# Optimization experiments

Hardware: AMD Instinct MI355X
Metric: run time of the kernel (lower is better)

## Reference

```python
import jax, jax.numpy as jnp
import numpy as np

IN_DIM = 1024
OUT_DIM = 1024


def setup_inputs() -> dict:
    key = jax.random.key(0)
    k1, k2, k3, k4 = jax.random.split(key, 4)
    B, T = 4, 2048
    x = jax.random.normal(k1, (B, T, IN_DIM), dtype=jnp.float32)
    # torch Linear stores weight as [out, in]; y = x @ W.T
    s = 1.0 / np.sqrt(IN_DIM)
    Wq = jax.random.uniform(k2, (OUT_DIM, IN_DIM), jnp.float32, -s, s)
    Wk = jax.random.uniform(k3, (OUT_DIM, IN_DIM), jnp.float32, -s, s)
    Wv = jax.random.uniform(k4, (OUT_DIM, IN_DIM), jnp.float32, -s, s)
    return {"x": x, "Wq": Wq, "Wk": Wk, "Wv": Wv}


def reference(x, Wq, Wk, Wv):
    # x: [B, T, D_in]
    q = jnp.einsum('btd,od->bto', x, Wq)   # [B, T, D_out]
    k = jnp.einsum('btd,od->bto', x, Wk)
    v = jnp.einsum('btd,od->bto', x, Wv)
    T = x.shape[1]
    scores = jnp.einsum('bqo,bko->bqk', q, k)  # [B, T, T]
    causal = jnp.tril(jnp.ones((T, T), dtype=bool))  # True = keep
    scores = jnp.where(causal, scores, -jnp.inf)
    scale = 1.0 / jnp.sqrt(jnp.asarray(k.shape[-1], scores.dtype))
    weights = jax.nn.softmax(scores * scale, axis=-1)
    # dropout_value = 0.0 -> identity
    return jnp.einsum('bqk,bko->bqo', weights, v)
```

## Files before the change

kernel.cpp:

```cpp
#include <hip/hip_runtime.h>
#include <cstdint>
#include <cstddef>

typedef __attribute__((ext_vector_type(8))) short bf16x8;
typedef __attribute__((ext_vector_type(4))) float f32x4;

#define CSCALE 0.045084220027780106f

__device__ __forceinline__ void gload_lds16(const void* g, void* l) {
  __builtin_amdgcn_global_load_lds(
      (const __attribute__((address_space(1))) unsigned int*)g,
      (__attribute__((address_space(3))) unsigned int*)l, 16, 0, 0);
}

__device__ __forceinline__ unsigned short f2bf(float f) {
  unsigned int u = __float_as_uint(f);
  return (unsigned short)((u + 0x7FFFu + ((u >> 16) & 1u)) >> 16);
}

__device__ __forceinline__ float bf2f(unsigned short u) {
  return __uint_as_float((unsigned int)u << 16);
}

__global__ void cvt_kernel(const float* __restrict__ in,
                           unsigned short* __restrict__ out, int n8) {
  int i = blockIdx.x * blockDim.x + threadIdx.x;
  if (i >= n8) return;
  const float4* p = (const float4*)in + (size_t)i * 2;
  float4 a = p[0], b = p[1];
  float vals[8] = {a.x, a.y, a.z, a.w, b.x, b.y, b.z, b.w};
  union { unsigned short u[8]; uint4 v; } r;
#pragma unroll
  for (int j = 0; j < 8; ++j) r.u[j] = f2bf(vals[j]);
  ((uint4*)out)[i] = r.v;
}

template <int MODE>
__global__ __launch_bounds__(256) void gemm_k(
    const unsigned short* __restrict__ A, const unsigned short* __restrict__ B,
    void* __restrict__ Cv) {
  constexpr int LDA = (MODE <= 1) ? 1024 : 2048;
  constexpr int LDB = (MODE <= 1) ? 1024 : (MODE == 2 ? 2048 : 8192);
  constexpr int LDC =
      (MODE == 0) ? 2048 : (MODE == 1 ? 8192 : (MODE == 2 ? 2048 : 1024));

  int arow, brow, ksteps = 32, kb = 0;
  size_t cbase;
  if constexpr (MODE == 0 || MODE == 1) {
    arow = blockIdx.x * 128;
    brow = blockIdx.y * 128;
    cbase = (size_t)arow * LDC + blockIdx.y * 128;
  } else if constexpr (MODE == 2) {
    int i = blockIdx.x, j = blockIdx.y, b = blockIdx.z;
    if (j > i) return;
    arow = b * 2048 + i * 128;
    brow = b * 2048 + j * 128;
    cbase = (size_t)(b * 2048 + i * 128) * LDC + j * 128;
  } else {
    int bm = blockIdx.x;
    int b = bm >> 4, qt = 15 - (bm & 15);
    arow = b * 2048 + qt * 128;
    brow = blockIdx.y * 128;
    kb = b * 2048;
    ksteps = (qt + 1) * 4;
    cbase = (size_t)(b * 2048 + qt * 128) * LDC + blockIdx.y * 128;
  }

  __shared__ unsigned short As[2][4096];
  __shared__ unsigned short Bs[2][4096];
  const int tid = threadIdx.x, w = tid >> 6, lane = tid & 63;
  const int l15 = lane & 15, g = lane >> 4;
  const int wm = w >> 1, wn = w & 1;
  f32x4 acc[4][4] = {};

  auto stage = [&](int buf, int k0) {
#pragma unroll
    for (int oi = 0; oi < 2; ++oi) {
      int o = w + oi * 4;
      int chunk = o * 64 + lane;
      int row = chunk >> 2, c8 = chunk & 3;
      gload_lds16(A + (size_t)(arow + row) * LDA + k0 + c8 * 8,
                  &As[buf][o * 512]);
      gload_lds16(B + (size_t)(brow + row) * LDB + kb + k0 + c8 * 8,
                  &Bs[buf][o * 512]);
    }
  };

  stage(0, 0);
  asm volatile("s_waitcnt vmcnt(0)" ::: "memory");
  __builtin_amdgcn_s_barrier();

  for (int t = 0; t < ksteps; ++t) {
    int buf = t & 1;
    if (t + 1 < ksteps) stage(buf ^ 1, (t + 1) * 32);
    bf16x8 af[4], bfr[4];
#pragma unroll
    for (int mt = 0; mt < 4; ++mt)
      af[mt] = *(const bf16x8*)&As[buf][(wm * 64 + mt * 16 + l15) * 32 + g * 8];
#pragma unroll
    for (int nt = 0; nt < 4; ++nt)
      bfr[nt] = *(const bf16x8*)&Bs[buf][(wn * 64 + nt * 16 + l15) * 32 + g * 8];
#pragma unroll
    for (int mt = 0; mt < 4; ++mt)
#pragma unroll
      for (int nt = 0; nt < 4; ++nt)
        acc[mt][nt] = __builtin_amdgcn_mfma_f32_16x16x32_bf16(
            af[mt], bfr[nt], acc[mt][nt], 0, 0, 0);
    asm volatile("s_waitcnt vmcnt(0)" ::: "memory");
    __builtin_amdgcn_s_barrier();
  }

#pragma unroll
  for (int mt = 0; mt < 4; ++mt) {
#pragma unroll
    for (int r = 0; r < 4; ++r) {
      int ro = wm * 64 + mt * 16 + g * 4 + r;
      int co = wn * 64 + l15;
      if constexpr (MODE == 3) {
        float* Cp = (float*)Cv + cbase + (size_t)ro * LDC + co;
#pragma unroll
        for (int nt = 0; nt < 4; ++nt) Cp[nt * 16] = acc[mt][nt][r];
      } else {
        unsigned short* Cp = (unsigned short*)Cv + cbase + (size_t)ro * LDC + co;
#pragma unroll
        for (int nt = 0; nt < 4; ++nt) Cp[nt * 16] = f2bf(acc[mt][nt][r]);
      }
    }
  }
}

__global__ __launch_bounds__(256) void softmax_kernel(
    unsigned short* __restrict__ S) {
  const int r = blockIdx.x * 4 + (threadIdx.x >> 6);
  const int lane = threadIdx.x & 63;
  const int q = r & 2047;
  unsigned short* row = S + (size_t)r * 2048;
  const int klen = q + 1;
  const int kmax = ((q >> 7) + 1) << 7;

  float v[4][8];
  float m = -__builtin_inff();
#pragma unroll
  for (int it = 0; it < 4; ++it) {
    int base = (lane + it * 64) * 8;
    if (base < klen) {
      bf16x8 u = *(const bf16x8*)(row + base);
#pragma unroll
      for (int e = 0; e < 8; ++e) {
        float f = bf2f((unsigned short)u[e]) * CSCALE;
        v[it][e] = (base + e <= q) ? f : -__builtin_inff();
        m = fmaxf(m, v[it][e]);
      }
    } else {
#pragma unroll
      for (int e = 0; e < 8; ++e) v[it][e] = -__builtin_inff();
    }
  }
#pragma unroll
  for (int s = 1; s < 64; s <<= 1) m = fmaxf(m, __shfl_xor(m, s));

  float lsum = 0.f;
#pragma unroll
  for (int it = 0; it < 4; ++it)
#pragma unroll
    for (int e = 0; e < 8; ++e) {
      float p = exp2f(v[it][e] - m);
      v[it][e] = p;
      lsum += p;
    }
#pragma unroll
  for (int s = 1; s < 64; s <<= 1) lsum += __shfl_xor(lsum, s);
  float inv = 1.0f / lsum;

#pragma unroll
  for (int it = 0; it < 4; ++it) {
    int base = (lane + it * 64) * 8;
    if (base < kmax) {
      union { unsigned short u[8]; uint4 x; } o;
#pragma unroll
      for (int e = 0; e < 8; ++e) o.u[e] = f2bf(v[it][e] * inv);
      *(uint4*)(row + base) = o.x;
    }
  }
}

extern "C" void kernel_launch(void* const* d_in, const int* in_sizes, int n_in,
                              void* d_out, int out_size, void* d_ws,
                              size_t ws_size, hipStream_t stream) {
  const float* x = (const float*)d_in[0];
  const float* Wq = (const float*)d_in[1];
  const float* Wk = (const float*)d_in[2];
  const float* Wv = (const float*)d_in[3];
  unsigned short* ws = (unsigned short*)d_ws;
  unsigned short* xb = ws;
  unsigned short* Wqk = ws + (size_t)(8u << 20);
  unsigned short* Wvb = ws + (size_t)(10u << 20);
  unsigned short* QKb = ws + (size_t)(11u << 20);
  unsigned short* Vtb = ws + (size_t)(27u << 20);
  unsigned short* Sb = ws + (size_t)(35u << 20);

  cvt_kernel<<<4096, 256, 0, stream>>>(x, xb, 1048576);
  cvt_kernel<<<512, 256, 0, stream>>>(Wq, Wqk, 131072);
  cvt_kernel<<<512, 256, 0, stream>>>(Wk, Wqk + (size_t)(1u << 20), 131072);
  cvt_kernel<<<512, 256, 0, stream>>>(Wv, Wvb, 131072);
  gemm_k<0><<<dim3(64, 16), 256, 0, stream>>>(xb, Wqk, QKb);
  gemm_k<1><<<dim3(8, 64), 256, 0, stream>>>(Wvb, xb, Vtb);
  gemm_k<2><<<dim3(16, 16, 4), 256, 0, stream>>>(QKb, QKb + 1024, Sb);
  softmax_kernel<<<2048, 256, 0, stream>>>(Sb);
  gemm_k<3><<<dim3(64, 8), 256, 0, stream>>>(Sb, Vtb, (float*)d_out);
}
```

Baseline: 286.7 us.

## Use 256x128 GEMM tiles with triple-buffered swizzled LDS and 8 waves

Replaces the 128x128, 4-wave, double-buffered GEMM with a 256x128 tile, 8 waves (512 threads), BK=64 and a 3-stage LDS pipeline. The LDS layout is XOR-swizzled to avoid bank conflicts, and global loads are interleaved with the MFMA phases under setprio and barriers. The three weight conversions are merged into one launch. Softmax now zero-fills up to a 256-column boundary to match the new causal tile granularity. The larger tiles cut global traffic per FLOP and hide load latency, at the cost of more wasted work on the causal diagonal and fewer blocks.

After: 259.4 us. 1.11x faster.

```diff
diff --git a/kernel.cpp b/kernel.cpp
--- a/kernel.cpp
+++ b/kernel.cpp
@@ -35,99 +35,187 @@
   ((uint4*)out)[i] = r.v;
 }
 
+__global__ void cvt3_kernel(const float* __restrict__ a,
+                            const float* __restrict__ b,
+                            const float* __restrict__ c,
+                            unsigned short* __restrict__ oa,
+                            unsigned short* __restrict__ ob,
+                            unsigned short* __restrict__ oc) {
+  int bid = blockIdx.x;
+  const float* src;
+  unsigned short* dst;
+  int base;
+  if (bid < 512) { src = a; dst = oa; base = bid; }
+  else if (bid < 1024) { src = b; dst = ob; base = bid - 512; }
+  else { src = c; dst = oc; base = bid - 1024; }
+  int i = base * 256 + threadIdx.x;
+  const float4* p = (const float4*)src + (size_t)i * 2;
+  float4 x = p[0], y = p[1];
+  float vals[8] = {x.x, x.y, x.z, x.w, y.x, y.y, y.z, y.w};
+  union { unsigned short u[8]; uint4 v; } r;
+#pragma unroll
+  for (int j = 0; j < 8; ++j) r.u[j] = f2bf(vals[j]);
+  ((uint4*)dst)[i] = r.v;
+}
+
 template <int MODE>
-__global__ __launch_bounds__(256) void gemm_k(
-    const unsigned short* __restrict__ A, const unsigned short* __restrict__ B,
-    void* __restrict__ Cv) {
+__device__ __forceinline__ void gemm8_body(const unsigned short* __restrict__ A,
+                                           const unsigned short* __restrict__ B,
+                                           void* __restrict__ Cv) {
   constexpr int LDA = (MODE <= 1) ? 1024 : 2048;
   constexpr int LDB = (MODE <= 1) ? 1024 : (MODE == 2 ? 2048 : 8192);
   constexpr int LDC =
       (MODE == 0) ? 2048 : (MODE == 1 ? 8192 : (MODE == 2 ? 2048 : 1024));
 
-  int arow, brow, ksteps = 32, kb = 0;
+  int arow, brow, nt = 16, kb = 0;
   size_t cbase;
   if constexpr (MODE == 0 || MODE == 1) {
-    arow = blockIdx.x * 128;
+    arow = blockIdx.x * 256;
     brow = blockIdx.y * 128;
     cbase = (size_t)arow * LDC + blockIdx.y * 128;
   } else if constexpr (MODE == 2) {
-    int i = blockIdx.x, j = blockIdx.y, b = blockIdx.z;
-    if (j > i) return;
-    arow = b * 2048 + i * 128;
-    brow = b * 2048 + j * 128;
-    cbase = (size_t)(b * 2048 + i * 128) * LDC + j * 128;
+    int qt = blockIdx.x, jt = blockIdx.y, b = blockIdx.z;
+    if (jt > 2 * qt + 1) return;
+    arow = b * 2048 + qt * 256;
+    brow = b * 2048 + jt * 128;
+    cbase = (size_t)arow * LDC + jt * 128;
   } else {
     int bm = blockIdx.x;
-    int b = bm >> 4, qt = 15 - (bm & 15);
-    arow = b * 2048 + qt * 128;
+    int b = bm >> 3, qt = 7 - (bm & 7);
+    arow = b * 2048 + qt * 256;
     brow = blockIdx.y * 128;
     kb = b * 2048;
-    ksteps = (qt + 1) * 4;
-    cbase = (size_t)(b * 2048 + qt * 128) * LDC + blockIdx.y * 128;
-  }
-
-  __shared__ unsigned short As[2][4096];
-  __shared__ unsigned short Bs[2][4096];
-  const int tid = threadIdx.x, w = tid >> 6, lane = tid & 63;
+    nt = (qt + 1) * 4;
+    cbase = (size_t)arow * LDC + blockIdx.y * 128;
+  }
+
+  __shared__ unsigned short As[3][256 * 64];
+  __shared__ unsigned short Bs[3][128 * 64];
+
+  const int tid = threadIdx.x;
+  const int lane = tid & 63;
   const int l15 = lane & 15, g = lane >> 4;
-  const int wm = w >> 1, wn = w & 1;
-  f32x4 acc[4][4] = {};
-
-  auto stage = [&](int buf, int k0) {
-#pragma unroll
-    for (int oi = 0; oi < 2; ++oi) {
-      int o = w + oi * 4;
-      int chunk = o * 64 + lane;
-      int row = chunk >> 2, c8 = chunk & 3;
-      gload_lds16(A + (size_t)(arow + row) * LDA + k0 + c8 * 8,
-                  &As[buf][o * 512]);
-      gload_lds16(B + (size_t)(brow + row) * LDB + kb + k0 + c8 * 8,
-                  &Bs[buf][o * 512]);
+  const int w = tid >> 6;
+  const int wm = w >> 2, wn = w & 3;
+
+  f32x4 acc[8][2] = {};
+
+  auto stage_op = [&](int buf, int t, int op) {
+    int k0 = t * 64;
+    if (op < 4) {
+      int chunk = op * 512 + tid;
+      int row = chunk >> 3, c8 = chunk & 7;
+      int ce = (c8 * 16) ^ ((row & 7) << 4);
+      gload_lds16(A + (size_t)(arow + row) * LDA + k0 + (ce >> 1),
+                  &As[buf][(op * 512 + (tid & ~63)) * 8]);
+    } else {
+      int chunk = (op - 4) * 512 + tid;
+      int row = chunk >> 3, c8 = chunk & 7;
+      int ce = (c8 * 16) ^ ((row & 7) << 4);
+      gload_lds16(B + (size_t)(brow + row) * LDB + kb + k0 + (ce >> 1),
+                  &Bs[buf][((op - 4) * 512 + (tid & ~63)) * 8]);
     }
   };
 
-  stage(0, 0);
-  asm volatile("s_waitcnt vmcnt(0)" ::: "memory");
+  auto lda_frag = [&](int buf, int mt, int kk) -> bf16x8 {
+    int row = wm * 128 + mt * 16 + l15;
+    int byte = (row * 128 + kk * 64 + g * 16) ^ ((l15 & 7) << 4);
+    return *(const bf16x8*)((const char*)&As[buf][0] + byte);
+  };
+  auto ldb_frag = [&](int buf, int n2, int kk) -> bf16x8 {
+    int row = wn * 32 + n2 * 16 + l15;
+    int byte = (row * 128 + kk * 64 + g * 16) ^ ((l15 & 7) << 4);
+    return *(const bf16x8*)((const char*)&Bs[buf][0] + byte);
+  };
+
+#pragma unroll
+  for (int op = 0; op < 6; ++op) stage_op(0, 0, op);
+#pragma unroll
+  for (int op = 0; op < 6; ++op) stage_op(1, 1, op);
+  asm volatile("s_waitcnt vmcnt(6)" ::: "memory");
   __builtin_amdgcn_s_barrier();
 
-  for (int t = 0; t < ksteps; ++t) {
-    int buf = t & 1;
-    if (t + 1 < ksteps) stage(buf ^ 1, (t + 1) * 32);
-    bf16x8 af[4], bfr[4];
-#pragma unroll
-    for (int mt = 0; mt < 4; ++mt)
-      af[mt] = *(const bf16x8*)&As[buf][(wm * 64 + mt * 16 + l15) * 32 + g * 8];
-#pragma unroll
-    for (int nt = 0; nt < 4; ++nt)
-      bfr[nt] = *(const bf16x8*)&Bs[buf][(wn * 64 + nt * 16 + l15) * 32 + g * 8];
-#pragma unroll
-    for (int mt = 0; mt < 4; ++mt)
-#pragma unroll
-      for (int nt = 0; nt < 4; ++nt)
-        acc[mt][nt] = __builtin_amdgcn_mfma_f32_16x16x32_bf16(
-            af[mt], bfr[nt], acc[mt][nt], 0, 0, 0);
-    asm volatile("s_waitcnt vmcnt(0)" ::: "memory");
-    __builtin_amdgcn_s_barrier();
-  }
-
-#pragma unroll
-  for (int mt = 0; mt < 4; ++mt) {
+  for (int t = 0; t < nt; ++t) {
+    int buf = t % 3;
+    int sbuf = (t + 2) % 3;
+    bool do_stage = (t + 2) < nt;
+#pragma unroll
+    for (int ph = 0; ph < 2; ++ph) {
+      bf16x8 af[4][2], bv[2][2];
+#pragma unroll
+      for (int mt = 0; mt < 4; ++mt)
+#pragma unroll
+        for (int kk = 0; kk < 2; ++kk)
+          af[mt][kk] = lda_frag(buf, ph * 4 + mt, kk);
+#pragma unroll
+      for (int n2 = 0; n2 < 2; ++n2)
+#pragma unroll
+        for (int kk = 0; kk < 2; ++kk) bv[n2][kk] = ldb_frag(buf, n2, kk);
+      if (do_stage) {
+        if (ph == 0) {
+          stage_op(sbuf, t + 2, 0);
+          stage_op(sbuf, t + 2, 1);
+          stage_op(sbuf, t + 2, 4);
+        } else {
+          stage_op(sbuf, t + 2, 2);
+          stage_op(sbuf, t + 2, 3);
+          stage_op(sbuf, t + 2, 5);
+        }
+      }
+      __builtin_amdgcn_s_barrier();
+      asm volatile("s_waitcnt lgkmcnt(0)" ::: "memory");
+      __builtin_amdgcn_sched_barrier(0);
+      __builtin_amdgcn_s_setprio(1);
+#pragma unroll
+      for (int mt = 0; mt < 4; ++mt)
+#pragma unroll
+        for (int n2 = 0; n2 < 2; ++n2)
+#pragma unroll
+          for (int kk = 0; kk < 2; ++kk)
+            acc[ph * 4 + mt][n2] = __builtin_amdgcn_mfma_f32_16x16x32_bf16(
+                af[mt][kk], bv[n2][kk], acc[ph * 4 + mt][n2], 0, 0, 0);
+      __builtin_amdgcn_s_setprio(0);
+      __builtin_amdgcn_s_barrier();
+    }
+    if (do_stage) {
+      asm volatile("s_waitcnt vmcnt(6)" ::: "memory");
+    } else if (t + 1 < nt) {
+      asm volatile("s_waitcnt vmcnt(0)" ::: "memory");
+    }
+  }
+
+#pragma unroll
+  for (int mt = 0; mt < 8; ++mt) {
 #pragma unroll
     for (int r = 0; r < 4; ++r) {
-      int ro = wm * 64 + mt * 16 + g * 4 + r;
-      int co = wn * 64 + l15;
+      int ro = wm * 128 + mt * 16 + g * 4 + r;
+      int co = wn * 32 + l15;
       if constexpr (MODE == 3) {
         float* Cp = (float*)Cv + cbase + (size_t)ro * LDC + co;
-#pragma unroll
-        for (int nt = 0; nt < 4; ++nt) Cp[nt * 16] = acc[mt][nt][r];
+        Cp[0] = acc[mt][0][r];
+        Cp[16] = acc[mt][1][r];
       } else {
-        unsigned short* Cp = (unsigned short*)Cv + cbase + (size_t)ro * LDC + co;
-#pragma unroll
-        for (int nt = 0; nt < 4; ++nt) Cp[nt * 16] = f2bf(acc[mt][nt][r]);
+        unsigned short* Cp =
+            (unsigned short*)Cv + cbase + (size_t)ro * LDC + co;
+        Cp[0] = f2bf(acc[mt][0][r]);
+        Cp[16] = f2bf(acc[mt][1][r]);
       }
     }
   }
 }
+
+__global__ __launch_bounds__(512) void gemm_proj(
+    const unsigned short* __restrict__ A, const unsigned short* __restrict__ B,
+    void* __restrict__ C) { gemm8_body<0>(A, B, C); }
+__global__ __launch_bounds__(512) void gemm_vt(
+    const unsigned short* __restrict__ A, const unsigned short* __restrict__ B,
+    void* __restrict__ C) { gemm8_body<1>(A, B, C); }
+__global__ __launch_bounds__(512) void gemm_s(
+    const unsigned short* __restrict__ A, const unsigned short* __restrict__ B,
+    void* __restrict__ C) { gemm8_body<2>(A, B, C); }
+__global__ __launch_bounds__(512) void gemm_pv(
+    const unsigned short* __restrict__ A, const unsigned short* __restrict__ B,
+    void* __restrict__ C) { gemm8_body<3>(A, B, C); }
 
 __global__ __launch_bounds__(256) void softmax_kernel(
     unsigned short* __restrict__ S) {
@@ -136,7 +224,7 @@
   const int q = r & 2047;
   unsigned short* row = S + (size_t)r * 2048;
   const int klen = q + 1;
-  const int kmax = ((q >> 7) + 1) << 7;
+  const int kmax = ((q >> 8) + 1) << 8;
 
   float v[4][8];
   float m = -__builtin_inff();
@@ -200,12 +288,11 @@
   unsigned short* Sb = ws + (size_t)(35u << 20);
 
   cvt_kernel<<<4096, 256, 0, stream>>>(x, xb, 1048576);
-  cvt_kernel<<<512, 256, 0, stream>>>(Wq, Wqk, 131072);
-  cvt_kernel<<<512, 256, 0, stream>>>(Wk, Wqk + (size_t)(1u << 20), 131072);
-  cvt_kernel<<<512, 256, 0, stream>>>(Wv, Wvb, 131072);
-  gemm_k<0><<<dim3(64, 16), 256, 0, stream>>>(xb, Wqk, QKb);
-  gemm_k<1><<<dim3(8, 64), 256, 0, stream>>>(Wvb, xb, Vtb);
-  gemm_k<2><<<dim3(16, 16, 4), 256, 0, stream>>>(QKb, QKb + 1024, Sb);
+  cvt3_kernel<<<1536, 256, 0, stream>>>(Wq, Wk, Wv, Wqk,
+                                        Wqk + (size_t)(1u << 20), Wvb);
+  gemm_proj<<<dim3(32, 16), 512, 0, stream>>>(xb, Wqk, QKb);
+  gemm_vt<<<dim3(4, 64), 512, 0, stream>>>(Wvb, xb, Vtb);
+  gemm_s<<<dim3(8, 16, 4), 512, 0, stream>>>(QKb, QKb + 1024, Sb);
   softmax_kernel<<<2048, 256, 0, stream>>>(Sb);
-  gemm_k<3><<<dim3(64, 8), 256, 0, stream>>>(Sb, Vtb, (float*)d_out);
-}
+  gemm_pv<<<dim3(32, 8), 512, 0, stream>>>(Sb, Vtb, (float*)d_out);
+}
```

## Deepen GEMM pipeline to 4-stage LDS ring with swizzled layout and interleaved MFMA

Applied to the files above, without the earlier changes.

Replaces the double-buffered GEMM main loop with a four-slot LDS ring that prefetches three k-steps ahead. Loads of A and B are split across two MFMA half-phases, with s_setprio and sched barriers around the MFMA blocks. It adds an XOR/row-permuted LDS layout to avoid bank conflicts and sets launch bounds for two blocks per CU. The three weight conversions are merged into one launch. The larger LDS footprint (64KB per block) and extra barriers per step may limit occupancy.

Measured after the change: 251.3 us. 12.4% less time.

```diff
diff --git a/kernel.cpp b/kernel.cpp
--- a/kernel.cpp
+++ b/kernel.cpp
@@ -35,79 +35,144 @@
   ((uint4*)out)[i] = r.v;
 }
 
+__global__ void cvt3_kernel(const float* __restrict__ a,
+                            const float* __restrict__ b,
+                            const float* __restrict__ c,
+                            unsigned short* __restrict__ oa,
+                            unsigned short* __restrict__ ob,
+                            unsigned short* __restrict__ oc) {
+  int bid = blockIdx.x;
+  const float* src;
+  unsigned short* dst;
+  int base;
+  if (bid < 512) { src = a; dst = oa; base = bid; }
+  else if (bid < 1024) { src = b; dst = ob; base = bid - 512; }
+  else { src = c; dst = oc; base = bid - 1024; }
+  int i = base * 256 + threadIdx.x;
+  const float4* p = (const float4*)src + (size_t)i * 2;
+  float4 x = p[0], y = p[1];
+  float vals[8] = {x.x, x.y, x.z, x.w, y.x, y.y, y.z, y.w};
+  union { unsigned short u[8]; uint4 v; } r;
+#pragma unroll
+  for (int j = 0; j < 8; ++j) r.u[j] = f2bf(vals[j]);
+  ((uint4*)dst)[i] = r.v;
+}
+
 template <int MODE>
-__global__ __launch_bounds__(256) void gemm_k(
-    const unsigned short* __restrict__ A, const unsigned short* __restrict__ B,
-    void* __restrict__ Cv) {
+__device__ __forceinline__ void gemm_body(const unsigned short* __restrict__ A,
+                                          const unsigned short* __restrict__ B,
+                                          void* __restrict__ Cv) {
   constexpr int LDA = (MODE <= 1) ? 1024 : 2048;
   constexpr int LDB = (MODE <= 1) ? 1024 : (MODE == 2 ? 2048 : 8192);
   constexpr int LDC =
       (MODE == 0) ? 2048 : (MODE == 1 ? 8192 : (MODE == 2 ? 2048 : 1024));
 
-  int arow, brow, ksteps = 32, kb = 0;
+  int arow, brow, NT = 32, kb = 0;
   size_t cbase;
   if constexpr (MODE == 0 || MODE == 1) {
     arow = blockIdx.x * 128;
     brow = blockIdx.y * 128;
     cbase = (size_t)arow * LDC + blockIdx.y * 128;
   } else if constexpr (MODE == 2) {
-    int i = blockIdx.x, j = blockIdx.y, b = blockIdx.z;
-    if (j > i) return;
-    arow = b * 2048 + i * 128;
-    brow = b * 2048 + j * 128;
-    cbase = (size_t)(b * 2048 + i * 128) * LDC + j * 128;
+    int qt = blockIdx.x, jt = blockIdx.y, b = blockIdx.z;
+    if (jt > qt) return;
+    arow = b * 2048 + qt * 128;
+    brow = b * 2048 + jt * 128;
+    cbase = (size_t)arow * LDC + jt * 128;
   } else {
-    int bm = blockIdx.x;
-    int b = bm >> 4, qt = 15 - (bm & 15);
+    int b = blockIdx.x >> 4, qt = 15 - (blockIdx.x & 15);
     arow = b * 2048 + qt * 128;
     brow = blockIdx.y * 128;
     kb = b * 2048;
-    ksteps = (qt + 1) * 4;
-    cbase = (size_t)(b * 2048 + qt * 128) * LDC + blockIdx.y * 128;
-  }
-
-  __shared__ unsigned short As[2][4096];
-  __shared__ unsigned short Bs[2][4096];
-  const int tid = threadIdx.x, w = tid >> 6, lane = tid & 63;
+    NT = (qt + 1) * 4;
+    cbase = (size_t)arow * LDC + blockIdx.y * 128;
+  }
+
+  __shared__ char lds[4][16384];
+  const int tid = threadIdx.x, lane = tid & 63;
   const int l15 = lane & 15, g = lane >> 4;
-  const int wm = w >> 1, wn = w & 1;
+  const int w = tid >> 6, wm = w >> 1, wn = w & 1;
+
   f32x4 acc[4][4] = {};
 
-  auto stage = [&](int buf, int k0) {
-#pragma unroll
-    for (int oi = 0; oi < 2; ++oi) {
-      int o = w + oi * 4;
-      int chunk = o * 64 + lane;
-      int row = chunk >> 2, c8 = chunk & 3;
-      gload_lds16(A + (size_t)(arow + row) * LDA + k0 + c8 * 8,
-                  &As[buf][o * 512]);
-      gload_lds16(B + (size_t)(brow + row) * LDB + kb + k0 + c8 * 8,
-                  &Bs[buf][o * 512]);
+  auto stageA = [&](int slot, int jt) {
+#pragma unroll
+    for (int h = 0; h < 2; ++h) {
+      int q = h * 256 + tid;
+      int prow = q >> 2;
+      int row = (prow & ~5) | ((prow & 1) << 2) | ((prow >> 2) & 1);
+      int c = (q & 3) ^ (row & 3);
+      gload_lds16(A + (size_t)(arow + row) * LDA + jt * 32 + c * 8,
+                  &lds[slot][(q & ~63) * 16]);
     }
   };
-
-  stage(0, 0);
-  asm volatile("s_waitcnt vmcnt(0)" ::: "memory");
+  auto stageB = [&](int slot, int jt) {
+#pragma unroll
+    for (int h = 0; h < 2; ++h) {
+      int q = h * 256 + tid;
+      int prow = q >> 2;
+      int row = (prow & ~5) | ((prow & 1) << 2) | ((prow >> 2) & 1);
+      int c = (q & 3) ^ (row & 3);
+      gload_lds16(B + (size_t)(brow + row) * LDB + kb + jt * 32 + c * 8,
+                  &lds[slot][8192 + (q & ~63) * 16]);
+    }
+  };
+  auto ldf = [&](int slot, int off, int r16) -> bf16x8 {
+    int row = r16 * 16 + l15;
+    int prow = (row & ~5) | ((row & 1) << 2) | ((row >> 2) & 1);
+    return *(const bf16x8*)&lds[slot]
+        [off + prow * 64 + (((g ^ row) & 3) << 4)];
+  };
+
+  stageA(0, 0); stageB(0, 0);
+  stageA(1, 1); stageB(1, 1);
+  stageA(2, 2); stageB(2, 2);
+  asm volatile("s_waitcnt vmcnt(8)" ::: "memory");
   __builtin_amdgcn_s_barrier();
 
-  for (int t = 0; t < ksteps; ++t) {
-    int buf = t & 1;
-    if (t + 1 < ksteps) stage(buf ^ 1, (t + 1) * 32);
-    bf16x8 af[4], bfr[4];
-#pragma unroll
-    for (int mt = 0; mt < 4; ++mt)
-      af[mt] = *(const bf16x8*)&As[buf][(wm * 64 + mt * 16 + l15) * 32 + g * 8];
-#pragma unroll
-    for (int nt = 0; nt < 4; ++nt)
-      bfr[nt] = *(const bf16x8*)&Bs[buf][(wn * 64 + nt * 16 + l15) * 32 + g * 8];
-#pragma unroll
-    for (int mt = 0; mt < 4; ++mt)
-#pragma unroll
-      for (int nt = 0; nt < 4; ++nt)
-        acc[mt][nt] = __builtin_amdgcn_mfma_f32_16x16x32_bf16(
-            af[mt], bfr[nt], acc[mt][nt], 0, 0, 0);
-    asm volatile("s_waitcnt vmcnt(0)" ::: "memory");
-    __builtin_amdgcn_s_barrier();
+  for (int j = 0; j < NT; ++j) {
+    int slot = j & 3, ss = (j + 3) & 3;
+    bool st = (j + 3) < NT;
+    bf16x8 af[4];
+#pragma unroll
+    for (int mt = 0; mt < 4; ++mt) af[mt] = ldf(slot, 0, wm * 4 + mt);
+    bf16x8 bv0 = ldf(slot, 8192, wn * 4 + 0);
+    bf16x8 bv1 = ldf(slot, 8192, wn * 4 + 1);
+    if (st) stageA(ss, j + 3);
+    __builtin_amdgcn_s_barrier();
+    asm volatile("s_waitcnt lgkmcnt(0)" ::: "memory");
+    __builtin_amdgcn_sched_barrier(0);
+    __builtin_amdgcn_s_setprio(1);
+#pragma unroll
+    for (int mt = 0; mt < 4; ++mt) {
+      acc[mt][0] =
+          __builtin_amdgcn_mfma_f32_16x16x32_bf16(af[mt], bv0, acc[mt][0], 0, 0, 0);
+      acc[mt][1] =
+          __builtin_amdgcn_mfma_f32_16x16x32_bf16(af[mt], bv1, acc[mt][1], 0, 0, 0);
+    }
+    __builtin_amdgcn_s_setprio(0);
+    __builtin_amdgcn_s_barrier();
+    bf16x8 bv2 = ldf(slot, 8192, wn * 4 + 2);
+    bf16x8 bv3 = ldf(slot, 8192, wn * 4 + 3);
+    if (st) stageB(ss, j + 3);
+    __builtin_amdgcn_s_barrier();
+    asm volatile("s_waitcnt lgkmcnt(0)" ::: "memory");
+    __builtin_amdgcn_sched_barrier(0);
+    __builtin_amdgcn_s_setprio(1);
+#pragma unroll
+    for (int mt = 0; mt < 4; ++mt) {
+      acc[mt][2] =
+          __builtin_amdgcn_mfma_f32_16x16x32_bf16(af[mt], bv2, acc[mt][2], 0, 0, 0);
+      acc[mt][3] =
+          __builtin_amdgcn_mfma_f32_16x16x32_bf16(af[mt], bv3, acc[mt][3], 0, 0, 0);
+    }
+    __builtin_amdgcn_s_setprio(0);
+    __builtin_amdgcn_s_barrier();
+    if (st) {
+      asm volatile("s_waitcnt vmcnt(4)" ::: "memory");
+    } else {
+      asm volatile("s_waitcnt vmcnt(0)" ::: "memory");
+    }
   }
 
 #pragma unroll
@@ -119,15 +184,28 @@
       if constexpr (MODE == 3) {
         float* Cp = (float*)Cv + cbase + (size_t)ro * LDC + co;
 #pragma unroll
-        for (int nt = 0; nt < 4; ++nt) Cp[nt * 16] = acc[mt][nt][r];
+        for (int n2 = 0; n2 < 4; ++n2) Cp[n2 * 16] = acc[mt][n2][r];
       } else {
         unsigned short* Cp = (unsigned short*)Cv + cbase + (size_t)ro * LDC + co;
 #pragma unroll
-        for (int nt = 0; nt < 4; ++nt) Cp[nt * 16] = f2bf(acc[mt][nt][r]);
+        for (int n2 = 0; n2 < 4; ++n2) Cp[n2 * 16] = f2bf(acc[mt][n2][r]);
       }
     }
   }
 }
+
+__global__ __launch_bounds__(256, 2) void gemm_proj(
+    const unsigned short* __restrict__ A, const unsigned short* __restrict__ B,
+    void* __restrict__ C) { gemm_body<0>(A, B, C); }
+__global__ __launch_bounds__(256, 2) void gemm_vt(
+    const unsigned short* __restrict__ A, const unsigned short* __restrict__ B,
+    void* __restrict__ C) { gemm_body<1>(A, B, C); }
+__global__ __launch_bounds__(256, 2) void gemm_s(
+    const unsigned short* __restrict__ A, const unsigned short* __restrict__ B,
+    void* __restrict__ C) { gemm_body<2>(A, B, C); }
+__global__ __launch_bounds__(256, 2) void gemm_pv(
+    const unsigned short* __restrict__ A, const unsigned short* __restrict__ B,
+    void* __restrict__ C) { gemm_body<3>(A, B, C); }
 
 __global__ __launch_bounds__(256) void softmax_kernel(
     unsigned short* __restrict__ S) {
@@ -200,12 +278,11 @@
   unsigned short* Sb = ws + (size_t)(35u << 20);
 
   cvt_kernel<<<4096, 256, 0, stream>>>(x, xb, 1048576);
-  cvt_kernel<<<512, 256, 0, stream>>>(Wq, Wqk, 131072);
-  cvt_kernel<<<512, 256, 0, stream>>>(Wk, Wqk + (size_t)(1u << 20), 131072);
-  cvt_kernel<<<512, 256, 0, stream>>>(Wv, Wvb, 131072);
-  gemm_k<0><<<dim3(64, 16), 256, 0, stream>>>(xb, Wqk, QKb);
-  gemm_k<1><<<dim3(8, 64), 256, 0, stream>>>(Wvb, xb, Vtb);
-  gemm_k<2><<<dim3(16, 16, 4), 256, 0, stream>>>(QKb, QKb + 1024, Sb);
+  cvt3_kernel<<<1536, 256, 0, stream>>>(Wq, Wk, Wv, Wqk,
+                                        Wqk + (size_t)(1u << 20), Wvb);
+  gemm_proj<<<dim3(64, 16), 256, 0, stream>>>(xb, Wqk, QKb);
+  gemm_vt<<<dim3(8, 64), 256, 0, stream>>>(Wvb, xb, Vtb);
+  gemm_s<<<dim3(16, 16, 4), 256, 0, stream>>>(QKb, QKb + 1024, Sb);
   softmax_kernel<<<2048, 256, 0, stream>>>(Sb);
-  gemm_k<3><<<dim3(64, 8), 256, 0, stream>>>(Sb, Vtb, (float*)d_out);
-}
+  gemm_pv<<<dim3(64, 8), 256, 0, stream>>>(Sb, Vtb, (float*)d_out);
+}
```
